# Kernel tuning notes

Hardware: AMD Instinct MI355X
Metric: run time of the kernel (lower is better)

Reference implementation:

```python
import jax, jax.numpy as jnp
import numpy as np

B, S, IN, OUT, H, M = 16, 512, 512, 512, 8, 4
HF = OUT // H  # head_feats = 64


def setup_inputs() -> dict:
    key = jax.random.key(0)
    ks = jax.random.split(key, 12)
    std = 0.02
    queries = jax.random.normal(ks[0], (B, S, IN), jnp.float32)
    keys = jax.random.normal(ks[1], (B, S, IN), jnp.float32)
    timespans = jax.random.uniform(ks[2], (B, S), jnp.float32)
    # causal mask tiled over heads*batch, matching [H*B, S, S] score shape
    attention_masks = jnp.broadcast_to(jnp.tril(jnp.ones((S, S), jnp.float32)), (H * B, S, S))
    event_marks = jax.random.uniform(ks[3], (H * B, 1, S, M), jnp.float32)
    Wq = std * jax.random.normal(ks[4], (IN, OUT), jnp.float32)
    Wk = std * jax.random.normal(ks[5], (IN, OUT), jnp.float32)
    Wv = std * jax.random.normal(ks[6], (IN, OUT), jnp.float32)
    Wt = std * jax.random.normal(ks[7], (IN, OUT), jnp.float32)
    Wi = std * jax.random.normal(ks[8], (HF + 1, M * HF), jnp.float32)  # fc_i weight
    bi = jnp.zeros((M * HF,), jnp.float32)                               # fc_i bias
    weight_i = std * jax.random.normal(ks[9], (M, HF), jnp.float32)
    scale_i = jnp.zeros((M,), jnp.float32)
    return {"queries": queries, "keys": keys, "timespans": timespans,
            "attention_masks": attention_masks, "event_marks": event_marks,
            "Wq": Wq, "Wk": Wk, "Wv": Wv, "Wt": Wt, "Wi": Wi, "bi": bi,
            "weight_i": weight_i, "scale_i": scale_i}


def reference(queries, keys, timespans, attention_masks, event_marks,
              Wq, Wk, Wv, Wt, Wi, bi, weight_i, scale_i):
    # torch's cat(chunk(X, H, dim=2), dim=0) == [B,S,H,HF] -> [H,B,S,HF] -> flat h*B+b
    def split_heads(X):
        return X.reshape(B, S, H, HF).transpose(2, 0, 1, 3)  # [H,B,S,HF]

    Q = split_heads(queries @ Wq)
    K = split_heads(keys @ Wk)
    V = split_heads(keys @ Wv)
    T = split_heads(keys @ Wt)

    scores = jnp.einsum('hbqf,hbkf->hbqk', Q, K) / jnp.sqrt(jnp.float32(OUT))
    mask = attention_masks.reshape(H, B, S, S)
    scores = jnp.where(mask == 0.0, jnp.float32(-2 ** 32 + 1), scores)
    attn = jax.nn.softmax(scores, axis=-1)  # [H,B,Sq,Sk]

    E = jnp.einsum('hbqk,hbkf->hbqf', attn, T)  # events fed to intensity net

    # --- Hawkes intensities ---
    ts = jnp.broadcast_to(timespans[None, :, :, None], (H, B, S, 1))
    mu = jax.nn.sigmoid(jnp.concatenate([E, ts], axis=-1) @ Wi + bi)  # [H,B,S,M*HF]
    mu = mu.reshape(H, B, S, M, HF)  # chunk over marks along feature dim
    scale = jnp.exp(scale_i)  # [M]
    lam = jnp.einsum('hbsmf,mf->hbsm', mu, weight_i) / scale
    lam = scale * jnp.log1p(jnp.exp(lam))  # scaled softplus, [H,B,S,M]

    # mark_inty[h,b,q,k] = sum_m lam[h,b,q,m] * event_marks[h,b,k,m]
    em = event_marks.reshape(H, B, S, M)
    mark_inty = jnp.einsum('hbqm,hbkm->hbqk', lam, em)

    out = jnp.einsum('hbqk,hbkf->hbqf', attn * mark_inty, V)
    out = out.transpose(1, 2, 0, 3).reshape(B, S, OUT) + queries[..., :OUT]
    all_mark_inty = lam.reshape(H * B, S, M)
    return out, all_mark_inty
```

## Files before the change

kernel.cpp:

```cpp
#include <hip/hip_runtime.h>
#include <math.h>

typedef __attribute__((ext_vector_type(8))) short short8;
typedef __attribute__((ext_vector_type(4))) float f32x4;

static __device__ __forceinline__ unsigned short f2bf(float f) {
  unsigned int u = __float_as_uint(f);
  u += 0x7FFFu + ((u >> 16) & 1u);
  return (unsigned short)(u >> 16);
}

static __device__ __forceinline__ void cp16(void* lds, const void* g) {
  __builtin_amdgcn_global_load_lds((const __attribute__((address_space(1))) void*)g,
                                   (__attribute__((address_space(3))) void*)lds,
                                   16, 0, 0);
}

__global__ __launch_bounds__(256) void convert_k(
    const float* __restrict__ qin, const float* __restrict__ kin,
    const float* __restrict__ Wq, const float* __restrict__ Wk,
    const float* __restrict__ Wv, const float* __restrict__ Wt,
    const float* __restrict__ Wi,
    unsigned short* __restrict__ qbf, unsigned short* __restrict__ kbf,
    unsigned short* __restrict__ Wb, unsigned short* __restrict__ WiF)
{
  __shared__ unsigned short tr[64 * 68];
  const int blk = blockIdx.x, tid = threadIdx.x;
  if (blk < 8192) {
    const float* src = (blk < 4096) ? qin : kin;
    unsigned short* dst = (blk < 4096) ? qbf : kbf;
    int i = ((blk & 4095) * 256 + tid) * 4;
    float4 v = *(const float4*)(src + i);
    ushort4 o;
    o.x = f2bf(v.x); o.y = f2bf(v.y); o.z = f2bf(v.z); o.w = f2bf(v.w);
    *(ushort4*)(dst + i) = o;
  } else if (blk < 8448) {
    int t = blk - 8192;
    int which = t >> 6, tile = t & 63;
    int r0 = (tile >> 3) << 6, c0 = (tile & 7) << 6;
    const float* W = (which == 0) ? Wq : (which == 1) ? Wk : (which == 2) ? Wv : Wt;
    const int rr = tid >> 4, cc = (tid & 15) << 2;
#pragma unroll
    for (int u = 0; u < 4; ++u) {
      int r = rr + u * 16;
      float4 v = *(const float4*)(W + (size_t)(r0 + r) * 512 + c0 + cc);
      tr[(cc + 0) * 68 + r] = f2bf(v.x);
      tr[(cc + 1) * 68 + r] = f2bf(v.y);
      tr[(cc + 2) * 68 + r] = f2bf(v.z);
      tr[(cc + 3) * 68 + r] = f2bf(v.w);
    }
    __syncthreads();
    unsigned short* dst = Wb + which * 262144;
#pragma unroll
    for (int u = 0; u < 4; ++u) {
      int c = rr + u * 16;
      ushort4 o = *(const ushort4*)&tr[c * 68 + cc];
      *(ushort4*)(dst + (size_t)(c0 + c) * 512 + r0 + cc) = o;
    }
  } else {
    int e = (blk - 8448) * 256 + tid;
    int j = e & 7, ll = (e >> 3) & 63, r = e >> 9;
    int kk = r % 3, nt = r / 3;
    int col = nt * 16 + (ll & 15);
    int k = kk * 32 + (ll >> 4) * 8 + j;
    float val = (k < 64) ? Wi[k * 256 + col] : ((k == 64) ? Wi[16384 + col] : 0.0f);
    WiF[e] = f2bf(val);
  }
}

__global__ __launch_bounds__(256) void proj_mfma(
    const unsigned short* __restrict__ qin_bf, const unsigned short* __restrict__ kin_bf,
    const unsigned short* __restrict__ Wb,
    unsigned short* __restrict__ Qg, unsigned short* __restrict__ Kg,
    unsigned short* __restrict__ Vt, unsigned short* __restrict__ Tt)
{
  const int which = blockIdx.z;
  const unsigned short* A = (which == 0) ? qin_bf : kin_bf;
  const unsigned short* W = Wb + which * 262144;
  const int row0 = blockIdx.x * 128;
  const int col0 = blockIdx.y * 128;
  const int tid = threadIdx.x;
  const int wv = tid >> 6, l = tid & 63;
  const int quad = l >> 4, lc = l & 15;
  const int wm = wv >> 1, wn = wv & 1;

  __shared__ unsigned short Asm[128 * 32];
  __shared__ unsigned short Bsm[128 * 32];

  f32x4 acc[4][4] = {};
  const int c0 = tid, c1 = tid + 256;

  for (int k0 = 0; k0 < 512; k0 += 32) {
    __syncthreads();
    cp16(&Asm[c0 * 8], A + (size_t)(row0 + (c0 >> 2)) * 512 + k0 + (c0 & 3) * 8);
    cp16(&Asm[c1 * 8], A + (size_t)(row0 + (c1 >> 2)) * 512 + k0 + (c1 & 3) * 8);
    cp16(&Bsm[c0 * 8], W + (size_t)(col0 + (c0 >> 2)) * 512 + k0 + (c0 & 3) * 8);
    cp16(&Bsm[c1 * 8], W + (size_t)(col0 + (c1 >> 2)) * 512 + k0 + (c1 & 3) * 8);
    __syncthreads();
    short8 a[4], b[4];
#pragma unroll
    for (int mi = 0; mi < 4; ++mi)
      a[mi] = *(const short8*)&Asm[(wm * 64 + mi * 16 + lc) * 32 + quad * 8];
#pragma unroll
    for (int nj = 0; nj < 4; ++nj)
      b[nj] = *(const short8*)&Bsm[(wn * 64 + nj * 16 + lc) * 32 + quad * 8];
#pragma unroll
    for (int mi = 0; mi < 4; ++mi)
#pragma unroll
      for (int nj = 0; nj < 4; ++nj)
        acc[mi][nj] = __builtin_amdgcn_mfma_f32_16x16x32_bf16(a[mi], b[nj], acc[mi][nj], 0, 0, 0);
  }

  const int h = (col0 >> 6) + wn;
  const int bidx = row0 >> 9;
  const int hb = h * 16 + bidx;
  if (which < 2) {
    unsigned short* C = (which == 0) ? Qg : Kg;
#pragma unroll
    for (int mi = 0; mi < 4; ++mi) {
      int sbase = (row0 & 511) + wm * 64 + mi * 16 + quad * 4;
#pragma unroll
      for (int nj = 0; nj < 4; ++nj) {
        size_t base = (size_t)hb * 32768 + (size_t)sbase * 64 + nj * 16 + lc;
#pragma unroll
        for (int reg = 0; reg < 4; ++reg)
          C[base + (size_t)reg * 64] = f2bf(acc[mi][nj][reg]);
      }
    }
  } else {
    unsigned short* C = (which == 2) ? Vt : Tt;
#pragma unroll
    for (int mi = 0; mi < 4; ++mi) {
      int sbase = (row0 & 511) + wm * 64 + mi * 16 + quad * 4;
#pragma unroll
      for (int nj = 0; nj < 4; ++nj) {
        ushort4 o;
        o.x = f2bf(acc[mi][nj][0]); o.y = f2bf(acc[mi][nj][1]);
        o.z = f2bf(acc[mi][nj][2]); o.w = f2bf(acc[mi][nj][3]);
        *(ushort4*)&C[(size_t)hb * 32768 + (size_t)(nj * 16 + lc) * 512 + sbase] = o;
      }
    }
  }
}

__global__ __launch_bounds__(256) void attn_fused(
    const unsigned short* __restrict__ Qg, const unsigned short* __restrict__ Kg,
    const unsigned short* __restrict__ Vtg, const unsigned short* __restrict__ Ttg,
    const unsigned short* __restrict__ WiF,
    const float* __restrict__ bi, const float* __restrict__ wim,
    const float* __restrict__ sci, const float* __restrict__ tsp,
    const float* __restrict__ em, const float* __restrict__ queries,
    float* __restrict__ out, float* __restrict__ lamout)
{
  const int hb = blockIdx.y;
  const int tid = threadIdx.x, wv = tid >> 6, l = tid & 63;
  const int quad = l >> 4, lc = l & 15;

  __shared__ unsigned short Qs[4096];
  __shared__ unsigned short Ks[4096];
  __shared__ unsigned short TVs[4096];
  __shared__ unsigned short Wl[4][16 * 104];
  __shared__ float emS[256];

  const float scl = 0.044194173824159216f;
  float scm[4];
#pragma unroll
  for (int m = 0; m < 4; ++m) scm[m] = __expf(sci[m]);

  for (int half = 0; half < 2; ++half) {
    const int qt = half ? (7 - blockIdx.x) : blockIdx.x;
    const int q0 = qt << 6;
    const int gqbase = q0 + wv * 16 + quad * 4;
    __syncthreads();
    const unsigned short* Qbase = Qg + (size_t)hb * 32768 + q0 * 64;
    cp16(&Qs[tid * 8], Qbase + tid * 8);
    cp16(&Qs[(tid + 256) * 8], Qbase + (tid + 256) * 8);

    f32x4 Eacc[4] = {};
    float lsum[4] = {0.f, 0.f, 0.f, 0.f};

    for (int kt = 0; kt <= qt; ++kt) {
      const int k0 = kt << 6;
      __syncthreads();
      const unsigned short* Kbase = Kg + (size_t)hb * 32768 + k0 * 64;
      cp16(&Ks[tid * 8], Kbase + tid * 8);
      cp16(&Ks[(tid + 256) * 8], Kbase + (tid + 256) * 8);
      const unsigned short* Tbase = Ttg + (size_t)hb * 32768 + k0;
      cp16(&TVs[tid * 8], Tbase + (size_t)(tid >> 3) * 512 + (tid & 7) * 8);
      cp16(&TVs[(tid + 256) * 8], Tbase + (size_t)((tid + 256) >> 3) * 512 + ((tid + 256) & 7) * 8);
      __syncthreads();

      f32x4 sc[4] = {};
#pragma unroll
      for (int kk = 0; kk < 2; ++kk) {
        short8 a = *(const short8*)&Qs[(wv * 16 + lc) * 64 + kk * 32 + quad * 8];
#pragma unroll
        for (int nj = 0; nj < 4; ++nj) {
          short8 b = *(const short8*)&Ks[(nj * 16 + lc) * 64 + kk * 32 + quad * 8];
          sc[nj] = __builtin_amdgcn_mfma_f32_16x16x32_bf16(a, b, sc[nj], 0, 0, 0);
        }
      }
      const bool diag = (kt == qt);
#pragma unroll
      for (int nj = 0; nj < 4; ++nj) {
        int col = nj * 16 + lc;
#pragma unroll
        for (int reg = 0; reg < 4; ++reg) {
          float pv = __expf(sc[nj][reg] * scl);
          if (diag && (k0 + col) > (gqbase + reg)) pv = 0.0f;
          lsum[reg] += pv;
          Wl[wv][(quad * 4 + reg) * 104 + col] = f2bf(pv);
        }
      }
#pragma unroll
      for (int kk = 0; kk < 2; ++kk) {
        short8 a = *(const short8*)&Wl[wv][lc * 104 + kk * 32 + quad * 8];
#pragma unroll
        for (int fj = 0; fj < 4; ++fj) {
          short8 b = *(const short8*)&TVs[(fj * 16 + lc) * 64 + kk * 32 + quad * 8];
          Eacc[fj] = __builtin_amdgcn_mfma_f32_16x16x32_bf16(a, b, Eacc[fj], 0, 0, 0);
        }
      }
    }

    float inv[4];
#pragma unroll
    for (int reg = 0; reg < 4; ++reg) {
      float s = lsum[reg];
#pragma unroll
      for (int off = 1; off < 16; off <<= 1) s += __shfl_xor(s, off);
      inv[reg] = 1.0f / s;
    }

#pragma unroll
    for (int reg = 0; reg < 4; ++reg) {
      unsigned short* rp = &Wl[wv][(quad * 4 + reg) * 104];
#pragma unroll
      for (int fj = 0; fj < 4; ++fj)
        rp[fj * 16 + lc] = f2bf(Eacc[fj][reg] * inv[reg]);
      float tsv = (lc == 0) ? tsp[(hb & 15) * 512 + gqbase + reg] : 0.0f;
      rp[64 + lc] = f2bf(tsv);
      rp[80 + lc] = 0;
    }

    f32x4 iacc[16] = {};
#pragma unroll
    for (int kk = 0; kk < 3; ++kk) {
      short8 a = *(const short8*)&Wl[wv][lc * 104 + kk * 32 + quad * 8];
#pragma unroll
      for (int nt = 0; nt < 16; ++nt) {
        short8 b = *(const short8*)(WiF + ((nt * 3 + kk) * 64 + l) * 8);
        iacc[nt] = __builtin_amdgcn_mfma_f32_16x16x32_bf16(a, b, iacc[nt], 0, 0, 0);
      }
    }
    float lam4[4][4] = {};
#pragma unroll
    for (int nt = 0; nt < 16; ++nt) {
      float bvv = bi[nt * 16 + lc];
      float wmv = wim[nt * 16 + lc];
#pragma unroll
      for (int reg = 0; reg < 4; ++reg) {
        float mu = 1.0f / (1.0f + __expf(-(iacc[nt][reg] + bvv)));
        lam4[reg][nt >> 2] += mu * wmv;
      }
    }
#pragma unroll
    for (int reg = 0; reg < 4; ++reg)
#pragma unroll
      for (int m = 0; m < 4; ++m) {
        float s = lam4[reg][m];
#pragma unroll
        for (int off = 1; off < 16; off <<= 1) s += __shfl_xor(s, off);
        float z = s / scm[m];
        float sp = (z > 20.0f) ? z : log1pf(__expf(z));
        lam4[reg][m] = scm[m] * sp;
      }
    if (lc < 4) {
#pragma unroll
      for (int reg = 0; reg < 4; ++reg) {
        float v = (lc == 0) ? lam4[reg][0] : (lc == 1) ? lam4[reg][1]
                : (lc == 2) ? lam4[reg][2] : lam4[reg][3];
        lamout[((size_t)hb * 512 + gqbase + reg) * 4 + lc] = v;
      }
    }

    f32x4 Oacc[4] = {};
    for (int kt = 0; kt <= qt; ++kt) {
      const int k0 = kt << 6;
      __syncthreads();
      const unsigned short* Kbase = Kg + (size_t)hb * 32768 + k0 * 64;
      cp16(&Ks[tid * 8], Kbase + tid * 8);
      cp16(&Ks[(tid + 256) * 8], Kbase + (tid + 256) * 8);
      const unsigned short* Vbase = Vtg + (size_t)hb * 32768 + k0;
      cp16(&TVs[tid * 8], Vbase + (size_t)(tid >> 3) * 512 + (tid & 7) * 8);
      cp16(&TVs[(tid + 256) * 8], Vbase + (size_t)((tid + 256) >> 3) * 512 + ((tid + 256) & 7) * 8);
      emS[tid] = em[(size_t)hb * 2048 + k0 * 4 + tid];
      __syncthreads();

      f32x4 sc[4] = {};
#pragma unroll
      for (int kk = 0; kk < 2; ++kk) {
        short8 a = *(const short8*)&Qs[(wv * 16 + lc) * 64 + kk * 32 + quad * 8];
#pragma unroll
        for (int nj = 0; nj < 4; ++nj) {
          short8 b = *(const short8*)&Ks[(nj * 16 + lc) * 64 + kk * 32 + quad * 8];
          sc[nj] = __builtin_amdgcn_mfma_f32_16x16x32_bf16(a, b, sc[nj], 0, 0, 0);
        }
      }
      const bool diag = (kt == qt);
#pragma unroll
      for (int nj = 0; nj < 4; ++nj) {
        int col = nj * 16 + lc;
        float4 emv = *(const float4*)&emS[col * 4];
#pragma unroll
        for (int reg = 0; reg < 4; ++reg) {
          float pv = (diag && (k0 + col) > (gqbase + reg))
                         ? 0.0f : __expf(sc[nj][reg] * scl) * inv[reg];
          float mk = lam4[reg][0] * emv.x + lam4[reg][1] * emv.y +
                     lam4[reg][2] * emv.z + lam4[reg][3] * emv.w;
          Wl[wv][(quad * 4 + reg) * 104 + col] = f2bf(pv * mk);
        }
      }
#pragma unroll
      for (int kk = 0; kk < 2; ++kk) {
        short8 a = *(const short8*)&Wl[wv][lc * 104 + kk * 32 + quad * 8];
#pragma unroll
        for (int fj = 0; fj < 4; ++fj) {
          short8 b = *(const short8*)&TVs[(fj * 16 + lc) * 64 + kk * 32 + quad * 8];
          Oacc[fj] = __builtin_amdgcn_mfma_f32_16x16x32_bf16(a, b, Oacc[fj], 0, 0, 0);
        }
      }
    }

    const int h = hb >> 4, bidx = hb & 15;
#pragma unroll
    for (int reg = 0; reg < 4; ++reg) {
      size_t o = (size_t)bidx * 262144 + (size_t)(gqbase + reg) * 512 + h * 64 + lc;
#pragma unroll
      for (int fj = 0; fj < 4; ++fj)
        out[o + fj * 16] = Oacc[fj][reg] + queries[o + fj * 16];
    }
  }
}

extern "C" void kernel_launch(void* const* d_in, const int* in_sizes, int n_in,
                              void* d_out, int out_size, void* d_ws, size_t ws_size,
                              hipStream_t stream)
{
  (void)in_sizes; (void)n_in; (void)out_size; (void)ws_size;
  const float* queries = (const float*)d_in[0];
  const float* keys    = (const float*)d_in[1];
  const float* tsp     = (const float*)d_in[2];
  const float* em      = (const float*)d_in[4];
  const float* Wq      = (const float*)d_in[5];
  const float* Wk      = (const float*)d_in[6];
  const float* Wv      = (const float*)d_in[7];
  const float* Wt      = (const float*)d_in[8];
  const float* Wi      = (const float*)d_in[9];
  const float* bi      = (const float*)d_in[10];
  const float* wim     = (const float*)d_in[11];
  const float* sci     = (const float*)d_in[12];
  float* out = (float*)d_out;

  char* w = (char*)d_ws;
  unsigned short* Qg     = (unsigned short*)(w + 0);
  unsigned short* Kg     = (unsigned short*)(w + 8388608);
  unsigned short* Vt     = (unsigned short*)(w + 16777216);
  unsigned short* Tt     = (unsigned short*)(w + 25165824);
  unsigned short* qin_bf = (unsigned short*)(w + 33554432);
  unsigned short* kin_bf = (unsigned short*)(w + 41943040);
  unsigned short* Wb     = (unsigned short*)(w + 50331648);
  unsigned short* WiF    = (unsigned short*)(w + 52428800);

  convert_k<<<8544, 256, 0, stream>>>(queries, keys, Wq, Wk, Wv, Wt, Wi,
                                      qin_bf, kin_bf, Wb, WiF);
  proj_mfma<<<dim3(64, 4, 4), 256, 0, stream>>>(qin_bf, kin_bf, Wb, Qg, Kg, Vt, Tt);
  attn_fused<<<dim3(4, 128), 256, 0, stream>>>(Qg, Kg, Vt, Tt, WiF, bi, wim, sci,
                                               tsp, em, queries, out,
                                               out + 4194304);
}
```

Measured before the change: 355.3 us.

## Swizzle LDS tiles, stage transposed stores via LDS, one q-tile per block

Applies XOR swizzling to the Q/K/T/V and weight LDS tiles to avoid bank conflicts. The transposed V/T epilogue of the projection kernel is staged through shared memory so global writes are contiguous 16-byte vectors. The attention kernel now handles one query tile per block on an 8x128 grid instead of pairing tiles for load balance, and raises occupancy with launch_bounds(256,3). The intensity MFMA loop is restructured to cut live accumulator registers. The risk is causal load imbalance across blocks.

```diff
diff --git a/kernel.cpp b/kernel.cpp
--- a/kernel.cpp
+++ b/kernel.cpp
@@ -129,21 +129,36 @@
     }
   } else {
     unsigned short* C = (which == 2) ? Vt : Tt;
-#pragma unroll
-    for (int mi = 0; mi < 4; ++mi) {
-      int sbase = (row0 & 511) + wm * 64 + mi * 16 + quad * 4;
-#pragma unroll
-      for (int nj = 0; nj < 4; ++nj) {
-        ushort4 o;
-        o.x = f2bf(acc[mi][nj][0]); o.y = f2bf(acc[mi][nj][1]);
-        o.z = f2bf(acc[mi][nj][2]); o.w = f2bf(acc[mi][nj][3]);
-        *(ushort4*)&C[(size_t)hb * 32768 + (size_t)(nj * 16 + lc) * 512 + sbase] = o;
-      }
-    }
-  }
-}
-
-__global__ __launch_bounds__(256) void attn_fused(
+    unsigned short* scr = wn ? Bsm : Asm;
+    const int sb = (row0 & 511) + wm * 64;
+    __syncthreads();
+#pragma unroll
+    for (int round = 0; round < 2; ++round) {
+      if (wm == round) {
+#pragma unroll
+        for (int mi = 0; mi < 4; ++mi)
+#pragma unroll
+          for (int nj = 0; nj < 4; ++nj)
+#pragma unroll
+            for (int reg = 0; reg < 4; ++reg) {
+              int f = nj * 16 + lc, s = mi * 16 + quad * 4 + reg;
+              int g = (s >> 3) ^ (f & 7);
+              scr[f * 64 + g * 8 + (s & 7)] = f2bf(acc[mi][nj][reg]);
+            }
+#pragma unroll
+        for (int it = 0; it < 8; ++it) {
+          int fl = it * 8 + (l >> 3);
+          int gg = (l & 7) ^ (fl & 7);
+          short8 v = *(const short8*)&scr[fl * 64 + gg * 8];
+          *(short8*)(C + (size_t)hb * 32768 + (size_t)fl * 512 + sb + (l & 7) * 8) = v;
+        }
+      }
+      __syncthreads();
+    }
+  }
+}
+
+__global__ __launch_bounds__(256, 3) void attn_fused(
     const unsigned short* __restrict__ Qg, const unsigned short* __restrict__ Kg,
     const unsigned short* __restrict__ Vtg, const unsigned short* __restrict__ Ttg,
     const unsigned short* __restrict__ WiF,
@@ -153,193 +168,205 @@
     float* __restrict__ out, float* __restrict__ lamout)
 {
   const int hb = blockIdx.y;
+  const int qt = 7 - blockIdx.x;
+  const int q0 = qt << 6;
   const int tid = threadIdx.x, wv = tid >> 6, l = tid & 63;
   const int quad = l >> 4, lc = l & 15;
+  const int xg = lc & 7;
 
   __shared__ unsigned short Qs[4096];
   __shared__ unsigned short Ks[4096];
   __shared__ unsigned short TVs[4096];
-  __shared__ unsigned short Wl[4][16 * 104];
+  __shared__ unsigned short Wl[4][1536];
   __shared__ float emS[256];
 
+  const int e1 = tid + 256;
+  const int sr0 = tid >> 3, sg0 = (tid & 7) ^ (sr0 & 7);
+  const int sr1 = e1 >> 3,  sg1 = (e1 & 7) ^ (sr1 & 7);
+  const int sqk0 = sr0 * 64 + sg0 * 8,  sqk1 = sr1 * 64 + sg1 * 8;
+  const int stv0 = sr0 * 512 + sg0 * 8, stv1 = sr1 * 512 + sg1 * 8;
+
   const float scl = 0.044194173824159216f;
-  float scm[4];
-#pragma unroll
-  for (int m = 0; m < 4; ++m) scm[m] = __expf(sci[m]);
-
-  for (int half = 0; half < 2; ++half) {
-    const int qt = half ? (7 - blockIdx.x) : blockIdx.x;
-    const int q0 = qt << 6;
-    const int gqbase = q0 + wv * 16 + quad * 4;
-    __syncthreads();
-    const unsigned short* Qbase = Qg + (size_t)hb * 32768 + q0 * 64;
-    cp16(&Qs[tid * 8], Qbase + tid * 8);
-    cp16(&Qs[(tid + 256) * 8], Qbase + (tid + 256) * 8);
-
-    f32x4 Eacc[4] = {};
-    float lsum[4] = {0.f, 0.f, 0.f, 0.f};
-
-    for (int kt = 0; kt <= qt; ++kt) {
-      const int k0 = kt << 6;
-      __syncthreads();
-      const unsigned short* Kbase = Kg + (size_t)hb * 32768 + k0 * 64;
-      cp16(&Ks[tid * 8], Kbase + tid * 8);
-      cp16(&Ks[(tid + 256) * 8], Kbase + (tid + 256) * 8);
-      const unsigned short* Tbase = Ttg + (size_t)hb * 32768 + k0;
-      cp16(&TVs[tid * 8], Tbase + (size_t)(tid >> 3) * 512 + (tid & 7) * 8);
-      cp16(&TVs[(tid + 256) * 8], Tbase + (size_t)((tid + 256) >> 3) * 512 + ((tid + 256) & 7) * 8);
-      __syncthreads();
-
-      f32x4 sc[4] = {};
-#pragma unroll
-      for (int kk = 0; kk < 2; ++kk) {
-        short8 a = *(const short8*)&Qs[(wv * 16 + lc) * 64 + kk * 32 + quad * 8];
-#pragma unroll
-        for (int nj = 0; nj < 4; ++nj) {
-          short8 b = *(const short8*)&Ks[(nj * 16 + lc) * 64 + kk * 32 + quad * 8];
-          sc[nj] = __builtin_amdgcn_mfma_f32_16x16x32_bf16(a, b, sc[nj], 0, 0, 0);
-        }
-      }
-      const bool diag = (kt == qt);
+  const int gqbase = q0 + wv * 16 + quad * 4;
+
+  const unsigned short* Qbase = Qg + (size_t)hb * 32768 + q0 * 64;
+  cp16(&Qs[tid * 8], Qbase + sqk0);
+  cp16(&Qs[e1 * 8], Qbase + sqk1);
+
+  f32x4 Eacc[4] = {};
+  float lsum[4] = {0.f, 0.f, 0.f, 0.f};
+
+  for (int kt = 0; kt <= qt; ++kt) {
+    const int k0 = kt << 6;
+    __syncthreads();
+    const unsigned short* Kbase = Kg + (size_t)hb * 32768 + k0 * 64;
+    cp16(&Ks[tid * 8], Kbase + sqk0);
+    cp16(&Ks[e1 * 8], Kbase + sqk1);
+    const unsigned short* Tbase = Ttg + (size_t)hb * 32768 + k0;
+    cp16(&TVs[tid * 8], Tbase + stv0);
+    cp16(&TVs[e1 * 8], Tbase + stv1);
+    __syncthreads();
+
+    f32x4 sc[4] = {};
+#pragma unroll
+    for (int kk = 0; kk < 2; ++kk) {
+      short8 a = *(const short8*)&Qs[(wv * 16 + lc) * 64 + ((kk * 4 + quad) ^ xg) * 8];
 #pragma unroll
       for (int nj = 0; nj < 4; ++nj) {
-        int col = nj * 16 + lc;
-#pragma unroll
-        for (int reg = 0; reg < 4; ++reg) {
-          float pv = __expf(sc[nj][reg] * scl);
-          if (diag && (k0 + col) > (gqbase + reg)) pv = 0.0f;
-          lsum[reg] += pv;
-          Wl[wv][(quad * 4 + reg) * 104 + col] = f2bf(pv);
-        }
-      }
-#pragma unroll
-      for (int kk = 0; kk < 2; ++kk) {
-        short8 a = *(const short8*)&Wl[wv][lc * 104 + kk * 32 + quad * 8];
-#pragma unroll
-        for (int fj = 0; fj < 4; ++fj) {
-          short8 b = *(const short8*)&TVs[(fj * 16 + lc) * 64 + kk * 32 + quad * 8];
-          Eacc[fj] = __builtin_amdgcn_mfma_f32_16x16x32_bf16(a, b, Eacc[fj], 0, 0, 0);
-        }
-      }
-    }
-
-    float inv[4];
+        short8 b = *(const short8*)&Ks[(nj * 16 + lc) * 64 + ((kk * 4 + quad) ^ xg) * 8];
+        sc[nj] = __builtin_amdgcn_mfma_f32_16x16x32_bf16(a, b, sc[nj], 0, 0, 0);
+      }
+    }
+    const bool diag = (kt == qt);
+#pragma unroll
+    for (int nj = 0; nj < 4; ++nj) {
+      int col = nj * 16 + lc;
+#pragma unroll
+      for (int reg = 0; reg < 4; ++reg) {
+        float pv = __expf(sc[nj][reg] * scl);
+        if (diag && (k0 + col) > (gqbase + reg)) pv = 0.0f;
+        lsum[reg] += pv;
+        int row = quad * 4 + reg;
+        int gp = (nj * 2 + (lc >> 3)) ^ (row & 7);
+        Wl[wv][row * 96 + gp * 8 + (lc & 7)] = f2bf(pv);
+      }
+    }
+#pragma unroll
+    for (int kk = 0; kk < 2; ++kk) {
+      short8 a = *(const short8*)&Wl[wv][lc * 96 + ((kk * 4 + quad) ^ xg) * 8];
+#pragma unroll
+      for (int fj = 0; fj < 4; ++fj) {
+        short8 b = *(const short8*)&TVs[(fj * 16 + lc) * 64 + ((kk * 4 + quad) ^ xg) * 8];
+        Eacc[fj] = __builtin_amdgcn_mfma_f32_16x16x32_bf16(a, b, Eacc[fj], 0, 0, 0);
+      }
+    }
+  }
+
+  float inv[4];
+#pragma unroll
+  for (int reg = 0; reg < 4; ++reg) {
+    float s = lsum[reg];
+#pragma unroll
+    for (int off = 1; off < 16; off <<= 1) s += __shfl_xor(s, off);
+    inv[reg] = 1.0f / s;
+  }
+
+#pragma unroll
+  for (int reg = 0; reg < 4; ++reg) {
+    int row = quad * 4 + reg;
+    unsigned short* rp = &Wl[wv][row * 96];
+#pragma unroll
+    for (int fj = 0; fj < 4; ++fj) {
+      int gp = (fj * 2 + (lc >> 3)) ^ (row & 7);
+      rp[gp * 8 + (lc & 7)] = f2bf(Eacc[fj][reg] * inv[reg]);
+    }
+    float tsv = (lc == 0) ? tsp[(hb & 15) * 512 + gqbase + reg] : 0.0f;
+    int gt = 8 + ((lc >> 3) ^ (row & 3));
+    rp[gt * 8 + (lc & 7)] = f2bf(tsv);
+    int gz = 8 + ((2 + (lc >> 3)) ^ (row & 3));
+    rp[gz * 8 + (lc & 7)] = 0;
+  }
+
+  short8 ia[3];
+  ia[0] = *(const short8*)&Wl[wv][lc * 96 + ((0 + quad) ^ xg) * 8];
+  ia[1] = *(const short8*)&Wl[wv][lc * 96 + ((4 + quad) ^ xg) * 8];
+  ia[2] = *(const short8*)&Wl[wv][lc * 96 + (8 + (quad ^ (lc & 3))) * 8];
+  float lam4[4][4] = {};
+#pragma unroll
+  for (int nt = 0; nt < 16; ++nt) {
+    f32x4 iacc = {};
+#pragma unroll
+    for (int kk = 0; kk < 3; ++kk) {
+      short8 b = *(const short8*)(WiF + ((nt * 3 + kk) * 64 + l) * 8);
+      iacc = __builtin_amdgcn_mfma_f32_16x16x32_bf16(ia[kk], b, iacc, 0, 0, 0);
+    }
+    float bvv = bi[nt * 16 + lc];
+    float wmv = wim[nt * 16 + lc];
 #pragma unroll
     for (int reg = 0; reg < 4; ++reg) {
-      float s = lsum[reg];
+      float mu = 1.0f / (1.0f + __expf(-(iacc[reg] + bvv)));
+      lam4[reg][nt >> 2] += mu * wmv;
+    }
+  }
+#pragma unroll
+  for (int m = 0; m < 4; ++m) {
+    float scv = __expf(sci[m]);
+#pragma unroll
+    for (int reg = 0; reg < 4; ++reg) {
+      float s = lam4[reg][m];
 #pragma unroll
       for (int off = 1; off < 16; off <<= 1) s += __shfl_xor(s, off);
-      inv[reg] = 1.0f / s;
-    }
-
+      float z = s / scv;
+      float sp = (z > 20.0f) ? z : log1pf(__expf(z));
+      lam4[reg][m] = scv * sp;
+    }
+  }
+  if (lc < 4) {
 #pragma unroll
     for (int reg = 0; reg < 4; ++reg) {
-      unsigned short* rp = &Wl[wv][(quad * 4 + reg) * 104];
-#pragma unroll
-      for (int fj = 0; fj < 4; ++fj)
-        rp[fj * 16 + lc] = f2bf(Eacc[fj][reg] * inv[reg]);
-      float tsv = (lc == 0) ? tsp[(hb & 15) * 512 + gqbase + reg] : 0.0f;
-      rp[64 + lc] = f2bf(tsv);
-      rp[80 + lc] = 0;
-    }
-
-    f32x4 iacc[16] = {};
-#pragma unroll
-    for (int kk = 0; kk < 3; ++kk) {
-      short8 a = *(const short8*)&Wl[wv][lc * 104 + kk * 32 + quad * 8];
-#pragma unroll
-      for (int nt = 0; nt < 16; ++nt) {
-        short8 b = *(const short8*)(WiF + ((nt * 3 + kk) * 64 + l) * 8);
-        iacc[nt] = __builtin_amdgcn_mfma_f32_16x16x32_bf16(a, b, iacc[nt], 0, 0, 0);
-      }
-    }
-    float lam4[4][4] = {};
-#pragma unroll
-    for (int nt = 0; nt < 16; ++nt) {
-      float bvv = bi[nt * 16 + lc];
-      float wmv = wim[nt * 16 + lc];
+      float v = (lc == 0) ? lam4[reg][0] : (lc == 1) ? lam4[reg][1]
+              : (lc == 2) ? lam4[reg][2] : lam4[reg][3];
+      lamout[((size_t)hb * 512 + gqbase + reg) * 4 + lc] = v;
+    }
+  }
+
+  f32x4 Oacc[4] = {};
+  for (int kt = 0; kt <= qt; ++kt) {
+    const int k0 = kt << 6;
+    __syncthreads();
+    const unsigned short* Kbase = Kg + (size_t)hb * 32768 + k0 * 64;
+    cp16(&Ks[tid * 8], Kbase + sqk0);
+    cp16(&Ks[e1 * 8], Kbase + sqk1);
+    const unsigned short* Vbase = Vtg + (size_t)hb * 32768 + k0;
+    cp16(&TVs[tid * 8], Vbase + stv0);
+    cp16(&TVs[e1 * 8], Vbase + stv1);
+    emS[tid] = em[(size_t)hb * 2048 + k0 * 4 + tid];
+    __syncthreads();
+
+    f32x4 sc[4] = {};
+#pragma unroll
+    for (int kk = 0; kk < 2; ++kk) {
+      short8 a = *(const short8*)&Qs[(wv * 16 + lc) * 64 + ((kk * 4 + quad) ^ xg) * 8];
+#pragma unroll
+      for (int nj = 0; nj < 4; ++nj) {
+        short8 b = *(const short8*)&Ks[(nj * 16 + lc) * 64 + ((kk * 4 + quad) ^ xg) * 8];
+        sc[nj] = __builtin_amdgcn_mfma_f32_16x16x32_bf16(a, b, sc[nj], 0, 0, 0);
+      }
+    }
+    const bool diag = (kt == qt);
+#pragma unroll
+    for (int nj = 0; nj < 4; ++nj) {
+      int col = nj * 16 + lc;
+      float4 emv = *(const float4*)&emS[col * 4];
 #pragma unroll
       for (int reg = 0; reg < 4; ++reg) {
-        float mu = 1.0f / (1.0f + __expf(-(iacc[nt][reg] + bvv)));
-        lam4[reg][nt >> 2] += mu * wmv;
-      }
-    }
-#pragma unroll
-    for (int reg = 0; reg < 4; ++reg)
-#pragma unroll
-      for (int m = 0; m < 4; ++m) {
-        float s = lam4[reg][m];
-#pragma unroll
-        for (int off = 1; off < 16; off <<= 1) s += __shfl_xor(s, off);
-        float z = s / scm[m];
-        float sp = (z > 20.0f) ? z : log1pf(__expf(z));
-        lam4[reg][m] = scm[m] * sp;
-      }
-    if (lc < 4) {
-#pragma unroll
-      for (int reg = 0; reg < 4; ++reg) {
-        float v = (lc == 0) ? lam4[reg][0] : (lc == 1) ? lam4[reg][1]
-                : (lc == 2) ? lam4[reg][2] : lam4[reg][3];
-        lamout[((size_t)hb * 512 + gqbase + reg) * 4 + lc] = v;
-      }
-    }
-
-    f32x4 Oacc[4] = {};
-    for (int kt = 0; kt <= qt; ++kt) {
-      const int k0 = kt << 6;
-      __syncthreads();
-      const unsigned short* Kbase = Kg + (size_t)hb * 32768 + k0 * 64;
-      cp16(&Ks[tid * 8], Kbase + tid * 8);
-      cp16(&Ks[(tid + 256) * 8], Kbase + (tid + 256) * 8);
-      const unsigned short* Vbase = Vtg + (size_t)hb * 32768 + k0;
-      cp16(&TVs[tid * 8], Vbase + (size_t)(tid >> 3) * 512 + (tid & 7) * 8);
-      cp16(&TVs[(tid + 256) * 8], Vbase + (size_t)((tid + 256) >> 3) * 512 + ((tid + 256) & 7) * 8);
-      emS[tid] = em[(size_t)hb * 2048 + k0 * 4 + tid];
-      __syncthreads();
-
-      f32x4 sc[4] = {};
-#pragma unroll
-      for (int kk = 0; kk < 2; ++kk) {
-        short8 a = *(const short8*)&Qs[(wv * 16 + lc) * 64 + kk * 32 + quad * 8];
-#pragma unroll
-        for (int nj = 0; nj < 4; ++nj) {
-          short8 b = *(const short8*)&Ks[(nj * 16 + lc) * 64 + kk * 32 + quad * 8];
-          sc[nj] = __builtin_amdgcn_mfma_f32_16x16x32_bf16(a, b, sc[nj], 0, 0, 0);
-        }
-      }
-      const bool diag = (kt == qt);
-#pragma unroll
-      for (int nj = 0; nj < 4; ++nj) {
-        int col = nj * 16 + lc;
-        float4 emv = *(const float4*)&emS[col * 4];
-#pragma unroll
-        for (int reg = 0; reg < 4; ++reg) {
-          float pv = (diag && (k0 + col) > (gqbase + reg))
-                         ? 0.0f : __expf(sc[nj][reg] * scl) * inv[reg];
-          float mk = lam4[reg][0] * emv.x + lam4[reg][1] * emv.y +
-                     lam4[reg][2] * emv.z + lam4[reg][3] * emv.w;
-          Wl[wv][(quad * 4 + reg) * 104 + col] = f2bf(pv * mk);
-        }
-      }
-#pragma unroll
-      for (int kk = 0; kk < 2; ++kk) {
-        short8 a = *(const short8*)&Wl[wv][lc * 104 + kk * 32 + quad * 8];
-#pragma unroll
-        for (int fj = 0; fj < 4; ++fj) {
-          short8 b = *(const short8*)&TVs[(fj * 16 + lc) * 64 + kk * 32 + quad * 8];
-          Oacc[fj] = __builtin_amdgcn_mfma_f32_16x16x32_bf16(a, b, Oacc[fj], 0, 0, 0);
-        }
-      }
-    }
-
-    const int h = hb >> 4, bidx = hb & 15;
-#pragma unroll
-    for (int reg = 0; reg < 4; ++reg) {
-      size_t o = (size_t)bidx * 262144 + (size_t)(gqbase + reg) * 512 + h * 64 + lc;
-#pragma unroll
-      for (int fj = 0; fj < 4; ++fj)
-        out[o + fj * 16] = Oacc[fj][reg] + queries[o + fj * 16];
-    }
+        float pv = (diag && (k0 + col) > (gqbase + reg))
+                       ? 0.0f : __expf(sc[nj][reg] * scl) * inv[reg];
+        float mk = lam4[reg][0] * emv.x + lam4[reg][1] * emv.y +
+                   lam4[reg][2] * emv.z + lam4[reg][3] * emv.w;
+        int row = quad * 4 + reg;
+        int gp = (nj * 2 + (lc >> 3)) ^ (row & 7);
+        Wl[wv][row * 96 + gp * 8 + (lc & 7)] = f2bf(pv * mk);
+      }
+    }
+#pragma unroll
+    for (int kk = 0; kk < 2; ++kk) {
+      short8 a = *(const short8*)&Wl[wv][lc * 96 + ((kk * 4 + quad) ^ xg) * 8];
+#pragma unroll
+      for (int fj = 0; fj < 4; ++fj) {
+        short8 b = *(const short8*)&TVs[(fj * 16 + lc) * 64 + ((kk * 4 + quad) ^ xg) * 8];
+        Oacc[fj] = __builtin_amdgcn_mfma_f32_16x16x32_bf16(a, b, Oacc[fj], 0, 0, 0);
+      }
+    }
+  }
+
+  const int h = hb >> 4, bidx = hb & 15;
+#pragma unroll
+  for (int reg = 0; reg < 4; ++reg) {
+    size_t o = (size_t)bidx * 262144 + (size_t)(gqbase + reg) * 512 + h * 64 + lc;
+#pragma unroll
+    for (int fj = 0; fj < 4; ++fj)
+      out[o + fj * 16] = Oacc[fj][reg] + queries[o + fj * 16];
   }
 }
 
@@ -375,7 +402,7 @@
   convert_k<<<8544, 256, 0, stream>>>(queries, keys, Wq, Wk, Wv, Wt, Wi,
                                       qin_bf, kin_bf, Wb, WiF);
   proj_mfma<<<dim3(64, 4, 4), 256, 0, stream>>>(qin_bf, kin_bf, Wb, Qg, Kg, Vt, Tt);
-  attn_fused<<<dim3(4, 128), 256, 0, stream>>>(Qg, Kg, Vt, Tt, WiF, bi, wim, sci,
+  attn_fused<<<dim3(8, 128), 256, 0, stream>>>(Qg, Kg, Vt, Tt, WiF, bi, wim, sci,
                                                tsp, em, queries, out,
                                                out + 4194304);
 }
```

Measured after the change: 323.8 us. -8.9%, faster.
